# Kernel tuning notes

Measured on AMD Instinct MI355X. Metric: run time of the kernel, lower is better.

Reference implementation:

```python
import jax, jax.numpy as jnp
import numpy as np

N_VOXELS = 150000
C = 128
NX = 400
NY = 400
B = 4


def setup_inputs() -> dict:
    key = jax.random.key(0)
    k1, k2, k3, k4 = jax.random.split(key, 4)
    voxel_features = jax.random.normal(k1, (N_VOXELS, C), dtype=jnp.float32)
    batch_idx = jax.random.randint(k2, (N_VOXELS,), 0, B, dtype=jnp.int64 if jax.config.jax_enable_x64 else jnp.int32)
    y_idx = jax.random.randint(k3, (N_VOXELS,), 0, NY, dtype=batch_idx.dtype)
    x_idx = jax.random.randint(k4, (N_VOXELS,), 0, NX, dtype=batch_idx.dtype)
    return {
        "voxel_features": voxel_features,
        "batch_idx": batch_idx,
        "y_idx": y_idx,
        "x_idx": x_idx,
        "batch_size": B,
    }


def reference(voxel_features, batch_idx, y_idx, x_idx, batch_size):
    # Fused scatter-amax: encode batch into the linear index so one segment_max
    # covers all batches (replaces the per-batch Python loop of the original).
    linear_idx = batch_idx * (NY * NX) + y_idx * NX + x_idx  # (N,)
    num_segments = batch_size * NY * NX
    # segment_max over voxels -> (B*NY*NX, C); empty cells come back as -inf
    seg = jax.ops.segment_max(voxel_features, linear_idx, num_segments=num_segments)
    # torch.scatter_reduce(..., include_self=False) leaves untouched cells at 0
    seg = jnp.where(jnp.isneginf(seg), jnp.zeros((), dtype=seg.dtype), seg)
    # (B, NY, NX, C) -> (B, C, NY, NX)
    spatial_features = seg.reshape(batch_size, NY, NX, C).transpose(0, 3, 1, 2)
    return spatial_features
```

## Files before the change

kernel.cpp:

```cpp
#include <hip/hip_runtime.h>

#define NXv    400
#define NYv    400
#define Bv     4
#define Cv     128
#define Sv     (NXv * NYv)
#define NCELLS (Bv * Sv)
#define TILE   64

__global__ __launch_bounds__(256) void build_lists_kernel(
        const int* __restrict__ batch_idx,
        const int* __restrict__ y_idx,
        const int* __restrict__ x_idx,
        int* __restrict__ head,
        int* __restrict__ nxt,
        int n_voxels) {
    int v = blockIdx.x * 256 + threadIdx.x;
    if (v >= n_voxels) return;
    int cell = batch_idx[v] * Sv + y_idx[v] * NXv + x_idx[v];
    int old = atomicExch(&head[cell], v);
    nxt[v] = old;
}

__global__ __launch_bounds__(256) void gather_max_kernel(
        const float4* __restrict__ feat4,
        const int* __restrict__ head,
        const int* __restrict__ nxt,
        float* __restrict__ out) {
    const int lane = threadIdx.x & 63;
    const int wave = threadIdx.x >> 6;
    const int cell0 = blockIdx.x * TILE;
    const int cell = cell0 + lane;
    const int b = cell0 / Sv;
    const int s = cell - b * Sv;
    const int h = head[cell];
    const int obase = b * (Cv * Sv) + s;

    #pragma unroll
    for (int j = 0; j < 8; ++j) {
        const int c4 = wave * 8 + j;
        float4 m = make_float4(-3.402823466e38f, -3.402823466e38f,
                               -3.402823466e38f, -3.402823466e38f);
        for (int v = h; v != -1; v = nxt[v]) {
            float4 f = feat4[v * (Cv / 4) + c4];
            m.x = fmaxf(m.x, f.x);
            m.y = fmaxf(m.y, f.y);
            m.z = fmaxf(m.z, f.z);
            m.w = fmaxf(m.w, f.w);
        }
        if (h == -1) {
            m = make_float4(0.f, 0.f, 0.f, 0.f);
        }
        const int c = c4 * 4;
        out[obase + (c + 0) * Sv] = m.x;
        out[obase + (c + 1) * Sv] = m.y;
        out[obase + (c + 2) * Sv] = m.z;
        out[obase + (c + 3) * Sv] = m.w;
    }
}

extern "C" void kernel_launch(void* const* d_in, const int* in_sizes, int n_in,
                              void* d_out, int out_size, void* d_ws, size_t ws_size,
                              hipStream_t stream) {
    const float* feat      = (const float*)d_in[0];
    const int*   batch_idx = (const int*)d_in[1];
    const int*   y_idx     = (const int*)d_in[2];
    const int*   x_idx     = (const int*)d_in[3];
    float* out = (float*)d_out;

    const int n_voxels = in_sizes[1];

    int* head = (int*)d_ws;
    int* nxt  = head + NCELLS;

    hipMemsetAsync(head, 0xFF, (size_t)NCELLS * sizeof(int), stream);

    build_lists_kernel<<<(n_voxels + 255) / 256, 256, 0, stream>>>(
        batch_idx, y_idx, x_idx, head, nxt, n_voxels);

    gather_max_kernel<<<NCELLS / TILE, 256, 0, stream>>>(
        (const float4*)feat, head, nxt, out);
}
```

Before: 444.7 us.

## Process four cells per thread with vectorized float4 transposed output stores

Each thread now handles four consecutive cells and a 16-channel band instead of one cell per eight channel groups. This lets it write float4 stores along the spatial dimension of the transposed output, and it walks each linked list once for all 16 channels rather than once per channel group. The head read becomes an int4 load and the tile grows to 128 cells per block. In exchange there are more registers per thread (64 accumulator floats) and more branch divergence across the four independent list walks.

Measured after the change: 413.7 us. 1.07x faster.

```diff
diff --git a/kernel.cpp b/kernel.cpp
--- a/kernel.cpp
+++ b/kernel.cpp
@@ -6,7 +6,9 @@
 #define Cv     128
 #define Sv     (NXv * NYv)
 #define NCELLS (Bv * Sv)
-#define TILE   64
+#define TILE   128
+
+#define NEG_FLT_MAX (-3.402823466e38f)
 
 __global__ __launch_bounds__(256) void build_lists_kernel(
         const int* __restrict__ batch_idx,
@@ -22,40 +24,78 @@
     nxt[v] = old;
 }
 
+__device__ __forceinline__ float4 fmax4(float4 a, float4 b) {
+    return make_float4(fmaxf(a.x, b.x), fmaxf(a.y, b.y),
+                       fmaxf(a.z, b.z), fmaxf(a.w, b.w));
+}
+
 __global__ __launch_bounds__(256) void gather_max_kernel(
         const float4* __restrict__ feat4,
-        const int* __restrict__ head,
-        const int* __restrict__ nxt,
-        float* __restrict__ out) {
-    const int lane = threadIdx.x & 63;
-    const int wave = threadIdx.x >> 6;
-    const int cell0 = blockIdx.x * TILE;
-    const int cell = cell0 + lane;
-    const int b = cell0 / Sv;
-    const int s = cell - b * Sv;
-    const int h = head[cell];
-    const int obase = b * (Cv * Sv) + s;
+        const int4*   __restrict__ head4,
+        const int*    __restrict__ nxt,
+        float4*       __restrict__ out4) {
+    const int sub   = threadIdx.x & 31;
+    const int band  = threadIdx.x >> 5;
+    const int tile0 = blockIdx.x * TILE;
+    const int b     = tile0 / Sv;
+    const int s0    = tile0 - b * Sv + sub * 4;
+    const int c4b   = band * 4;
 
+    const int4 h = head4[blockIdx.x * (TILE / 4) + sub];
+    int v0 = h.x, v1 = h.y, v2 = h.z, v3 = h.w;
+
+    float4 a0[4], a1[4], a2[4], a3[4];
     #pragma unroll
-    for (int j = 0; j < 8; ++j) {
-        const int c4 = wave * 8 + j;
-        float4 m = make_float4(-3.402823466e38f, -3.402823466e38f,
-                               -3.402823466e38f, -3.402823466e38f);
-        for (int v = h; v != -1; v = nxt[v]) {
-            float4 f = feat4[v * (Cv / 4) + c4];
-            m.x = fmaxf(m.x, f.x);
-            m.y = fmaxf(m.y, f.y);
-            m.z = fmaxf(m.z, f.z);
-            m.w = fmaxf(m.w, f.w);
+    for (int k = 0; k < 4; ++k) {
+        a0[k] = a1[k] = a2[k] = a3[k] =
+            make_float4(NEG_FLT_MAX, NEG_FLT_MAX, NEG_FLT_MAX, NEG_FLT_MAX);
+    }
+
+    while ((v0 >= 0) | (v1 >= 0) | (v2 >= 0) | (v3 >= 0)) {
+        if (v0 >= 0) {
+            const float4* __restrict__ r = feat4 + (size_t)v0 * (Cv / 4) + c4b;
+            const int vn = nxt[v0];
+            a0[0] = fmax4(a0[0], r[0]); a0[1] = fmax4(a0[1], r[1]);
+            a0[2] = fmax4(a0[2], r[2]); a0[3] = fmax4(a0[3], r[3]);
+            v0 = vn;
         }
-        if (h == -1) {
-            m = make_float4(0.f, 0.f, 0.f, 0.f);
+        if (v1 >= 0) {
+            const float4* __restrict__ r = feat4 + (size_t)v1 * (Cv / 4) + c4b;
+            const int vn = nxt[v1];
+            a1[0] = fmax4(a1[0], r[0]); a1[1] = fmax4(a1[1], r[1]);
+            a1[2] = fmax4(a1[2], r[2]); a1[3] = fmax4(a1[3], r[3]);
+            v1 = vn;
         }
-        const int c = c4 * 4;
-        out[obase + (c + 0) * Sv] = m.x;
-        out[obase + (c + 1) * Sv] = m.y;
-        out[obase + (c + 2) * Sv] = m.z;
-        out[obase + (c + 3) * Sv] = m.w;
+        if (v2 >= 0) {
+            const float4* __restrict__ r = feat4 + (size_t)v2 * (Cv / 4) + c4b;
+            const int vn = nxt[v2];
+            a2[0] = fmax4(a2[0], r[0]); a2[1] = fmax4(a2[1], r[1]);
+            a2[2] = fmax4(a2[2], r[2]); a2[3] = fmax4(a2[3], r[3]);
+            v2 = vn;
+        }
+        if (v3 >= 0) {
+            const float4* __restrict__ r = feat4 + (size_t)v3 * (Cv / 4) + c4b;
+            const int vn = nxt[v3];
+            a3[0] = fmax4(a3[0], r[0]); a3[1] = fmax4(a3[1], r[1]);
+            a3[2] = fmax4(a3[2], r[2]); a3[3] = fmax4(a3[3], r[3]);
+            v3 = vn;
+        }
+    }
+
+    const float4 z4 = make_float4(0.f, 0.f, 0.f, 0.f);
+    if (h.x < 0) { a0[0] = a0[1] = a0[2] = a0[3] = z4; }
+    if (h.y < 0) { a1[0] = a1[1] = a1[2] = a1[3] = z4; }
+    if (h.z < 0) { a2[0] = a2[1] = a2[2] = a2[3] = z4; }
+    if (h.w < 0) { a3[0] = a3[1] = a3[2] = a3[3] = z4; }
+
+    const int obase = b * (Cv * (Sv / 4)) + (s0 >> 2);
+    #pragma unroll
+    for (int k = 0; k < 4; ++k) {
+        const int c0 = (c4b + k) * 4;
+        out4[obase + (c0 + 0) * (Sv / 4)] = make_float4(a0[k].x, a1[k].x, a2[k].x, a3[k].x);
+        out4[obase + (c0 + 1) * (Sv / 4)] = make_float4(a0[k].y, a1[k].y, a2[k].y, a3[k].y);
+        out4[obase + (c0 + 2) * (Sv / 4)] = make_float4(a0[k].z, a1[k].z, a2[k].z, a3[k].z);
+        out4[obase + (c0 + 3) * (Sv / 4)] = make_float4(a0[k].w, a1[k].w, a2[k].w, a3[k].w);
     }
 }
 
@@ -79,5 +119,5 @@
         batch_idx, y_idx, x_idx, head, nxt, n_voxels);
 
     gather_max_kernel<<<NCELLS / TILE, 256, 0, stream>>>(
-        (const float4*)feat, head, nxt, out);
+        (const float4*)feat, (const int4*)head, nxt, (float4*)out);
 }
```
